# Optimization experiments

Hardware: AMD Instinct MI355X
Metric: run time of the kernel (lower is better)

Reference implementation:

```python
import jax, jax.numpy as jnp
import numpy as np

REWARD_SCALE = 1.0
DIST_NORM = 2
LATENT_DIST_THRESHOLD = 6.0

BS, N_VIEWS, N_PART, F_DIM = 128, 4, 1024, 10


def setup_inputs() -> dict:
    key = jax.random.key(0)
    k1, k2, k3, k4 = jax.random.split(key, 4)
    achieved_goal = jax.random.normal(k1, (BS, N_VIEWS, N_PART, F_DIM), jnp.float32)
    desired_goal = jax.random.normal(k2, (BS, N_VIEWS, N_PART, F_DIM), jnp.float32)
    norm_mean = jax.random.normal(k3, (F_DIM,), jnp.float32)
    norm_std = jax.random.uniform(k4, (F_DIM,), jnp.float32, minval=0.5, maxval=1.5)
    return {"achieved_goal": achieved_goal, "desired_goal": desired_goal,
            "norm_mean": norm_mean, "norm_std": norm_std}


def _pairwise_sqdist(x, y):
    # x: [bs, n, d], y: [bs, m, d] -> [bs, n, m] squared L2 ('l2_simple')
    xx = jnp.sum(x * x, axis=-1)            # [bs, n]
    yy = jnp.sum(y * y, axis=-1)            # [bs, m]
    xy = jnp.einsum('bnd,bmd->bnm', x, y)   # [bs, n, m]
    return xx[:, :, None] + yy[:, None, :] - 2.0 * xy


def _particle_mask(particles):
    # latent_classifier is None -> obj_class_cond = ones -> mask = (1 == 0) = all False
    obj_on = particles[..., -1]
    return jnp.zeros_like(obj_on, dtype=bool)


def reference(achieved_goal, desired_goal, norm_mean, norm_std):
    # unnormalize (particle_normalizer.unnormalize modeled as affine)
    state_particles = achieved_goal * norm_std + norm_mean
    goal_particles = desired_goal * norm_std + norm_mean
    bs, n_views, n_particles, _ = state_particles.shape

    state_mask = _particle_mask(state_particles)   # [bs, nv, np] bool
    goal_mask = _particle_mask(goal_particles)

    # P_mask[b,v,i,j] = state_mask[b,v,i] | goal_mask[b,v,j]
    P_mask = jnp.logical_or(state_mask[..., :, None], goal_mask[..., None, :])

    state_vis = state_particles[..., 5:9]
    state_xy = state_particles[..., :2]
    goal_vis = goal_particles[..., 5:9]
    goal_xy = goal_particles[..., :2]

    inf = jnp.asarray(jnp.inf, state_particles.dtype)
    rewards = []
    for i in range(n_views):
        sxy = state_xy[:, i]                 # [bs, np, 2]
        gxy = goal_xy[:, i]
        gmask_i = goal_mask[:, i]            # [bs, np]
        smask_i = state_mask[:, i]

        P = _pairwise_sqdist(state_vis[:, i], goal_vis[:, i])  # [bs, np_state, np_goal]
        P = jnp.where(P_mask[:, i], inf, P)

        # goal -> state direction: min over state dim (axis 1)
        min_d1 = jnp.min(P, axis=1)                            # [bs, np_goal]
        idx1 = jnp.argmin(P, axis=1)                           # [bs, np_goal]
        d_goal = jnp.take_along_axis(sxy, idx1[..., None], axis=1)  # [bs, np_goal, 2]
        xy_dist_1 = jnp.linalg.norm(gxy - d_goal, ord=DIST_NORM, axis=-1)
        xy_dist_1 = jnp.where(min_d1 > LATENT_DIST_THRESHOLD, 1.0, xy_dist_1)
        xy_dist_1 = jnp.where(gmask_i, 0.0, xy_dist_1)
        n_obj_g = jnp.maximum(jnp.sum(~gmask_i, axis=1), 1)
        reward_g2s = -jnp.sum(xy_dist_1, axis=1) / n_obj_g

        # state -> goal direction: min over goal dim (axis 2)
        min_d2 = jnp.min(P, axis=2)
        idx2 = jnp.argmin(P, axis=2)
        d_state = jnp.take_along_axis(gxy, idx2[..., None], axis=1)
        xy_dist_2 = jnp.linalg.norm(sxy - d_state, ord=DIST_NORM, axis=-1)
        xy_dist_2 = jnp.where(min_d2 > LATENT_DIST_THRESHOLD, 1.0, xy_dist_2)
        xy_dist_2 = jnp.where(smask_i, 0.0, xy_dist_2)
        n_obj_s = jnp.maximum(jnp.sum(~smask_i, axis=1), 1)
        reward_s2g = -jnp.sum(xy_dist_2, axis=1) / n_obj_s

        rv = (reward_g2s + reward_s2g) / 2.0
        no_valid = jnp.logical_or(jnp.all(gmask_i, axis=-1), jnp.all(smask_i, axis=-1))
        rv = jnp.where(no_valid, -1.0, rv)
        rewards.append(rv)

    reward = jnp.mean(jnp.stack(rewards, axis=0), axis=0)   # [bs]
    return REWARD_SCALE * reward[:, None]                    # [bs, 1]
```

## Files before the change

### kernel.cpp

```cpp
#include <hip/hip_runtime.h>
#include <cstdint>
#include <cstddef>

#define NP    1024
#define FD    10
#define NV    4
#define BSZ   128
#define NSET  1024
#define TPB   256
#define RPT   2

#define OFF_CS 16777216

typedef float fv4 __attribute__((ext_vector_type(4)));
typedef const fv4 __attribute__((address_space(4)))* c4p;


extern "C" __global__ __launch_bounds__(256)
void chamfer_stage(const float* __restrict__ ag, const float* __restrict__ dg,
                   const float* __restrict__ nmean, const float* __restrict__ nstd,
                   float* __restrict__ vis2o, float* __restrict__ cso)
{
    __shared__ float raw[NP * FD];
    const int s   = blockIdx.x;
    const int tid = threadIdx.x;
    const float4* src = (const float4*)(((s & 1) ? ag : dg) + (size_t)(s >> 1) * (NP * FD));
    float4* lraw = (float4*)raw;
#pragma unroll
    for (int i = 0; i < 10; ++i)
        lraw[tid + 256 * i] = src[tid + 256 * i];

    float st0 = -2.0f * nstd[5], mn0 = -2.0f * nmean[5];
    float st1 = -2.0f * nstd[6], mn1 = -2.0f * nmean[6];
    float st2 = -2.0f * nstd[7], mn2 = -2.0f * nmean[7];
    float st3 = -2.0f * nstd[8], mn3 = -2.0f * nmean[8];
    __syncthreads();

    fv4*   vout = (fv4*)vis2o + (size_t)s * NP;
    float* cout = cso + (size_t)s * NP;
    for (int n = tid; n < NP; n += 256) {
        float v0 = fmaf(raw[FD * n + 5], st0, mn0);
        float v1 = fmaf(raw[FD * n + 6], st1, mn1);
        float v2 = fmaf(raw[FD * n + 7], st2, mn2);
        float v3 = fmaf(raw[FD * n + 8], st3, mn3);
        fv4 v; v.x = v0; v.y = v1; v.z = v2; v.w = v3;
        vout[n] = v;
        cout[n] = 0.25f * (v0 * v0 + v1 * v1 + v2 * v2 + v3 * v3);
    }
}

extern "C" __global__ __launch_bounds__(TPB, 8)
void chamfer_pairs(const float* __restrict__ vis2, const float* __restrict__ cs,
                   const float* __restrict__ ag, const float* __restrict__ dg,
                   const float* __restrict__ nmean, const float* __restrict__ nstd,
                   float* __restrict__ out )
{
    __shared__ float redbuf[TPB / 64];

    const int bid  = blockIdx.x;
    const int pd   = bid >> 1;
    const int half = bid & 1;
    const int pair = pd >> 1;
    const int d    = pd & 1;
    const int tid  = threadIdx.x;

    c4p cvisS = (c4p)(uintptr_t)(vis2 + (size_t)pd * NP * 4);
    c4p ccsS  = (c4p)(uintptr_t)(cs   + (size_t)pd * NP);
    const float4* cvisV = (const float4*)(vis2 + (size_t)pd * NP * 4);
    const float*  ccsV  = cs + (size_t)pd * NP;
    const float4* rvis4 = (const float4*)(vis2 + (size_t)(pd ^ 1) * NP * 4);
    const float*  rcs   = cs + (size_t)(pd ^ 1) * NP;

    const float* rxyg = ((d == 0) ? ag : dg) + (size_t)pair * (NP * FD);
    const float* cxyg = ((d == 0) ? dg : ag) + (size_t)pair * (NP * FD);

    float4 rv[RPT];
    float  rthr[RPT];
    float  bestd[RPT];
    int    bblk[RPT];
#pragma unroll
    for (int r = 0; r < RPT; ++r) {
        int n = half * 512 + tid + TPB * r;
        float4 t = rvis4[n];
        rv[r] = make_float4(-0.5f * t.x, -0.5f * t.y, -0.5f * t.z, -0.5f * t.w);
        rthr[r] = 6.0f - rcs[n];
        bestd[r] = 3.0e38f;
        bblk[r]  = 0;
    }

    for (int mb8 = 0; mb8 < NP / 8; ++mb8) {
        const int m = mb8 * 8;
        fv4 c0 = cvisS[m + 0];
        fv4 c1 = cvisS[m + 1];
        fv4 c2 = cvisS[m + 2];
        fv4 c3 = cvisS[m + 3];
        fv4 c4 = cvisS[m + 4];
        fv4 c5 = cvisS[m + 5];
        fv4 c6 = cvisS[m + 6];
        fv4 c7 = cvisS[m + 7];
        fv4 csA = ccsS[mb8 * 2 + 0];
        fv4 csB = ccsS[mb8 * 2 + 1];
#pragma unroll
        for (int r = 0; r < RPT; ++r) {
            float4 v = rv[r];
            float d0 = fmaf(v.x, c0.x, csA.x); d0 = fmaf(v.y, c0.y, d0); d0 = fmaf(v.z, c0.z, d0); d0 = fmaf(v.w, c0.w, d0);
            float d1 = fmaf(v.x, c1.x, csA.y); d1 = fmaf(v.y, c1.y, d1); d1 = fmaf(v.z, c1.z, d1); d1 = fmaf(v.w, c1.w, d1);
            float d2 = fmaf(v.x, c2.x, csA.z); d2 = fmaf(v.y, c2.y, d2); d2 = fmaf(v.z, c2.z, d2); d2 = fmaf(v.w, c2.w, d2);
            float d3 = fmaf(v.x, c3.x, csA.w); d3 = fmaf(v.y, c3.y, d3); d3 = fmaf(v.z, c3.z, d3); d3 = fmaf(v.w, c3.w, d3);
            float d4 = fmaf(v.x, c4.x, csB.x); d4 = fmaf(v.y, c4.y, d4); d4 = fmaf(v.z, c4.z, d4); d4 = fmaf(v.w, c4.w, d4);
            float d5 = fmaf(v.x, c5.x, csB.y); d5 = fmaf(v.y, c5.y, d5); d5 = fmaf(v.z, c5.z, d5); d5 = fmaf(v.w, c5.w, d5);
            float d6 = fmaf(v.x, c6.x, csB.z); d6 = fmaf(v.y, c6.y, d6); d6 = fmaf(v.z, c6.z, d6); d6 = fmaf(v.w, c6.w, d6);
            float d7 = fmaf(v.x, c7.x, csB.w); d7 = fmaf(v.y, c7.y, d7); d7 = fmaf(v.z, c7.z, d7); d7 = fmaf(v.w, c7.w, d7);
            float p0 = fminf(fminf(d0, d1), d2);
            float p1 = fminf(fminf(d3, d4), d5);
            float p2 = fminf(d6, d7);
            float bm = fminf(fminf(p0, p1), p2);
            bool lt = bm < bestd[r];
            bestd[r] = fminf(bestd[r], bm);
            bblk[r]  = lt ? m : bblk[r];
        }
    }

    const float std0 = nstd[0], mean0 = nmean[0];
    const float std1 = nstd[1], mean1 = nmean[1];
    float sum = 0.0f;
#pragma unroll
    for (int r = 0; r < RPT; ++r) {
        int n  = half * 512 + tid + TPB * r;
        int mb = bblk[r];
        float4 v = rv[r];
        float cse[8];
#pragma unroll
        for (int j = 0; j < 8; ++j) cse[j] = ccsV[mb + j];
        float dd[8];
#pragma unroll
        for (int j = 0; j < 8; ++j) {
            float4 c = cvisV[mb + j];
            float t = fmaf(v.x, c.x, cse[j]);
            t = fmaf(v.y, c.y, t);
            t = fmaf(v.z, c.z, t);
            t = fmaf(v.w, c.w, t);
            dd[j] = t;
        }
        int sel = 0;
#pragma unroll
        for (int j = 7; j >= 0; --j)
            if (dd[j] == bestd[r]) sel = j;
        int idx = mb + sel;

        float gx = fmaf(cxyg[(size_t)idx * FD + 0], std0, mean0);
        float gy = fmaf(cxyg[(size_t)idx * FD + 1], std1, mean1);
        float ax = fmaf(rxyg[(size_t)n * FD + 0], std0, mean0);
        float ay = fmaf(rxyg[(size_t)n * FD + 1], std1, mean1);
        float dx = ax - gx;
        float dy = ay - gy;
        float dist = sqrtf(dx * dx + dy * dy);
        if (bestd[r] > rthr[r]) dist = 1.0f;
        sum += dist;
    }

    for (int o = 32; o > 0; o >>= 1) sum += __shfl_down(sum, o, 64);
    if ((tid & 63) == 0) redbuf[tid >> 6] = sum;
    __syncthreads();
    if (tid == 0) {
        float s = redbuf[0] + redbuf[1] + redbuf[2] + redbuf[3];
        atomicAdd(&out[pair >> 2], s * (-1.0f / 8192.0f));
    }
}

extern "C" void kernel_launch(void* const* d_in, const int* in_sizes, int n_in,
                              void* d_out, int out_size, void* d_ws, size_t ws_size,
                              hipStream_t stream)
{
    const float* ag = (const float*)d_in[0];
    const float* dg = (const float*)d_in[1];
    const float* nm = (const float*)d_in[2];
    const float* ns = (const float*)d_in[3];

    char*  ws    = (char*)d_ws;
    float* vis2  = (float*)(ws);
    float* csbuf = (float*)(ws + OFF_CS);

    hipMemsetAsync(d_out, 0, BSZ * sizeof(float), stream);
    chamfer_stage<<<NSET, 256, 0, stream>>>(ag, dg, nm, ns, vis2, csbuf);
    chamfer_pairs<<<NSET * 2, TPB, 0, stream>>>(vis2, csbuf, ag, dg, nm, ns, (float*)d_out);
}
```

Baseline: 256.7 us.

## Fuse staging into pair kernel with LDS SoA columns and packed FMA

Drops the separate staging kernel and its workspace round trip. Each block now unnormalizes the column set into LDS in structure-of-arrays form and computes the row vectors directly from the inputs. The inner loop uses 2-wide vector FMA and min, which could map to packed fp32 instructions. The launch shape also changes: 128-thread blocks with 8 rows per thread and 1024 blocks, down from 2048. This cuts the number of blocks and removes the scalar-constant-load path, at the cost of redundant column preprocessing per block and lower occupancy.

```diff
diff --git a/kernel.cpp b/kernel.cpp
--- a/kernel.cpp
+++ b/kernel.cpp
@@ -2,77 +2,48 @@
 #include <cstdint>
 #include <cstddef>
 
-#define NP    1024
-#define FD    10
-#define NV    4
-#define BSZ   128
-#define NSET  1024
-#define TPB   256
-#define RPT   2
+#define NP  1024
+#define FD  10
+#define NV  4
+#define BSZ 128
+#define TPB 128
+#define RPT 8
 
-#define OFF_CS 16777216
+typedef float v2f __attribute__((ext_vector_type(2)));
+typedef float v4f __attribute__((ext_vector_type(4)));
 
-typedef float fv4 __attribute__((ext_vector_type(4)));
-typedef const fv4 __attribute__((address_space(4)))* c4p;
-
-
-extern "C" __global__ __launch_bounds__(256)
-void chamfer_stage(const float* __restrict__ ag, const float* __restrict__ dg,
-                   const float* __restrict__ nmean, const float* __restrict__ nstd,
-                   float* __restrict__ vis2o, float* __restrict__ cso)
-{
-    __shared__ float raw[NP * FD];
-    const int s   = blockIdx.x;
-    const int tid = threadIdx.x;
-    const float4* src = (const float4*)(((s & 1) ? ag : dg) + (size_t)(s >> 1) * (NP * FD));
-    float4* lraw = (float4*)raw;
-#pragma unroll
-    for (int i = 0; i < 10; ++i)
-        lraw[tid + 256 * i] = src[tid + 256 * i];
-
-    float st0 = -2.0f * nstd[5], mn0 = -2.0f * nmean[5];
-    float st1 = -2.0f * nstd[6], mn1 = -2.0f * nmean[6];
-    float st2 = -2.0f * nstd[7], mn2 = -2.0f * nmean[7];
-    float st3 = -2.0f * nstd[8], mn3 = -2.0f * nmean[8];
-    __syncthreads();
-
-    fv4*   vout = (fv4*)vis2o + (size_t)s * NP;
-    float* cout = cso + (size_t)s * NP;
-    for (int n = tid; n < NP; n += 256) {
-        float v0 = fmaf(raw[FD * n + 5], st0, mn0);
-        float v1 = fmaf(raw[FD * n + 6], st1, mn1);
-        float v2 = fmaf(raw[FD * n + 7], st2, mn2);
-        float v3 = fmaf(raw[FD * n + 8], st3, mn3);
-        fv4 v; v.x = v0; v.y = v1; v.z = v2; v.w = v3;
-        vout[n] = v;
-        cout[n] = 0.25f * (v0 * v0 + v1 * v1 + v2 * v2 + v3 * v3);
-    }
-}
-
-extern "C" __global__ __launch_bounds__(TPB, 8)
-void chamfer_pairs(const float* __restrict__ vis2, const float* __restrict__ cs,
-                   const float* __restrict__ ag, const float* __restrict__ dg,
+extern "C" __global__ __launch_bounds__(TPB, 2)
+void chamfer_pairs(const float* __restrict__ ag, const float* __restrict__ dg,
                    const float* __restrict__ nmean, const float* __restrict__ nstd,
                    float* __restrict__ out )
 {
-    __shared__ float redbuf[TPB / 64];
+    __shared__ float cxF[NP], cyF[NP], czF[NP], cwF[NP], csF[NP];
+    __shared__ float red[TPB / 64];
 
     const int bid  = blockIdx.x;
-    const int pd   = bid >> 1;
-    const int half = bid & 1;
-    const int pair = pd >> 1;
-    const int d    = pd & 1;
+    const int pair = bid >> 1;
+    const int d    = bid & 1;
     const int tid  = threadIdx.x;
 
-    c4p cvisS = (c4p)(uintptr_t)(vis2 + (size_t)pd * NP * 4);
-    c4p ccsS  = (c4p)(uintptr_t)(cs   + (size_t)pd * NP);
-    const float4* cvisV = (const float4*)(vis2 + (size_t)pd * NP * 4);
-    const float*  ccsV  = cs + (size_t)pd * NP;
-    const float4* rvis4 = (const float4*)(vis2 + (size_t)(pd ^ 1) * NP * 4);
-    const float*  rcs   = cs + (size_t)(pd ^ 1) * NP;
+    const float* rowsrc = ((d == 0) ? ag : dg) + (size_t)pair * (NP * FD);
+    const float* colsrc = ((d == 0) ? dg : ag) + (size_t)pair * (NP * FD);
 
-    const float* rxyg = ((d == 0) ? ag : dg) + (size_t)pair * (NP * FD);
-    const float* cxyg = ((d == 0) ? dg : ag) + (size_t)pair * (NP * FD);
+    const float s5 = -2.0f * nstd[5], m5 = -2.0f * nmean[5];
+    const float s6 = -2.0f * nstd[6], m6 = -2.0f * nmean[6];
+    const float s7 = -2.0f * nstd[7], m7 = -2.0f * nmean[7];
+    const float s8 = -2.0f * nstd[8], m8 = -2.0f * nmean[8];
+    const float std0 = nstd[0], mean0 = nmean[0];
+    const float std1 = nstd[1], mean1 = nmean[1];
+
+    for (int m = tid; m < NP; m += TPB) {
+        const float* p = colsrc + (size_t)m * FD;
+        float t0 = fmaf(p[5], s5, m5);
+        float t1 = fmaf(p[6], s6, m6);
+        float t2 = fmaf(p[7], s7, m7);
+        float t3 = fmaf(p[8], s8, m8);
+        cxF[m] = t0; cyF[m] = t1; czF[m] = t2; cwF[m] = t3;
+        csF[m] = 0.25f * (t0 * t0 + t1 * t1 + t2 * t2 + t3 * t3);
+    }
 
     float4 rv[RPT];
     float  rthr[RPT];
@@ -80,66 +51,79 @@
     int    bblk[RPT];
 #pragma unroll
     for (int r = 0; r < RPT; ++r) {
-        int n = half * 512 + tid + TPB * r;
-        float4 t = rvis4[n];
-        rv[r] = make_float4(-0.5f * t.x, -0.5f * t.y, -0.5f * t.z, -0.5f * t.w);
-        rthr[r] = 6.0f - rcs[n];
+        int n = tid + TPB * r;
+        const float* p = rowsrc + (size_t)n * FD;
+        float t0 = fmaf(p[5], s5, m5);
+        float t1 = fmaf(p[6], s6, m6);
+        float t2 = fmaf(p[7], s7, m7);
+        float t3 = fmaf(p[8], s8, m8);
+        rv[r] = make_float4(-0.5f * t0, -0.5f * t1, -0.5f * t2, -0.5f * t3);
+        float rss = 0.25f * (t0 * t0 + t1 * t1 + t2 * t2 + t3 * t3);
+        rthr[r] = 6.0f - rss;
         bestd[r] = 3.0e38f;
         bblk[r]  = 0;
     }
+    __syncthreads();
 
-    for (int mb8 = 0; mb8 < NP / 8; ++mb8) {
-        const int m = mb8 * 8;
-        fv4 c0 = cvisS[m + 0];
-        fv4 c1 = cvisS[m + 1];
-        fv4 c2 = cvisS[m + 2];
-        fv4 c3 = cvisS[m + 3];
-        fv4 c4 = cvisS[m + 4];
-        fv4 c5 = cvisS[m + 5];
-        fv4 c6 = cvisS[m + 6];
-        fv4 c7 = cvisS[m + 7];
-        fv4 csA = ccsS[mb8 * 2 + 0];
-        fv4 csB = ccsS[mb8 * 2 + 1];
+    const v4f* X4 = (const v4f*)cxF;
+    const v4f* Y4 = (const v4f*)cyF;
+    const v4f* Z4 = (const v4f*)czF;
+    const v4f* W4 = (const v4f*)cwF;
+    const v4f* S4 = (const v4f*)csF;
+
+#pragma unroll 2
+    for (int g = 0; g < NP / 8; ++g) {
+        const int m = g * 8;
+        v4f xA = X4[2 * g], xB = X4[2 * g + 1];
+        v4f yA = Y4[2 * g], yB = Y4[2 * g + 1];
+        v4f zA = Z4[2 * g], zB = Z4[2 * g + 1];
+        v4f wA = W4[2 * g], wB = W4[2 * g + 1];
+        v4f cA = S4[2 * g], cB = S4[2 * g + 1];
 #pragma unroll
         for (int r = 0; r < RPT; ++r) {
-            float4 v = rv[r];
-            float d0 = fmaf(v.x, c0.x, csA.x); d0 = fmaf(v.y, c0.y, d0); d0 = fmaf(v.z, c0.z, d0); d0 = fmaf(v.w, c0.w, d0);
-            float d1 = fmaf(v.x, c1.x, csA.y); d1 = fmaf(v.y, c1.y, d1); d1 = fmaf(v.z, c1.z, d1); d1 = fmaf(v.w, c1.w, d1);
-            float d2 = fmaf(v.x, c2.x, csA.z); d2 = fmaf(v.y, c2.y, d2); d2 = fmaf(v.z, c2.z, d2); d2 = fmaf(v.w, c2.w, d2);
-            float d3 = fmaf(v.x, c3.x, csA.w); d3 = fmaf(v.y, c3.y, d3); d3 = fmaf(v.z, c3.z, d3); d3 = fmaf(v.w, c3.w, d3);
-            float d4 = fmaf(v.x, c4.x, csB.x); d4 = fmaf(v.y, c4.y, d4); d4 = fmaf(v.z, c4.z, d4); d4 = fmaf(v.w, c4.w, d4);
-            float d5 = fmaf(v.x, c5.x, csB.y); d5 = fmaf(v.y, c5.y, d5); d5 = fmaf(v.z, c5.z, d5); d5 = fmaf(v.w, c5.w, d5);
-            float d6 = fmaf(v.x, c6.x, csB.z); d6 = fmaf(v.y, c6.y, d6); d6 = fmaf(v.z, c6.z, d6); d6 = fmaf(v.w, c6.w, d6);
-            float d7 = fmaf(v.x, c7.x, csB.w); d7 = fmaf(v.y, c7.y, d7); d7 = fmaf(v.z, c7.z, d7); d7 = fmaf(v.w, c7.w, d7);
-            float p0 = fminf(fminf(d0, d1), d2);
-            float p1 = fminf(fminf(d3, d4), d5);
-            float p2 = fminf(d6, d7);
-            float bm = fminf(fminf(p0, p1), p2);
+            v2f vx = {rv[r].x, rv[r].x};
+            v2f vy = {rv[r].y, rv[r].y};
+            v2f vz = {rv[r].z, rv[r].z};
+            v2f vw = {rv[r].w, rv[r].w};
+            v2f q0 = __builtin_elementwise_fma(vx, xA.lo, cA.lo);
+            q0 = __builtin_elementwise_fma(vy, yA.lo, q0);
+            q0 = __builtin_elementwise_fma(vz, zA.lo, q0);
+            q0 = __builtin_elementwise_fma(vw, wA.lo, q0);
+            v2f q1 = __builtin_elementwise_fma(vx, xA.hi, cA.hi);
+            q1 = __builtin_elementwise_fma(vy, yA.hi, q1);
+            q1 = __builtin_elementwise_fma(vz, zA.hi, q1);
+            q1 = __builtin_elementwise_fma(vw, wA.hi, q1);
+            v2f q2 = __builtin_elementwise_fma(vx, xB.lo, cB.lo);
+            q2 = __builtin_elementwise_fma(vy, yB.lo, q2);
+            q2 = __builtin_elementwise_fma(vz, zB.lo, q2);
+            q2 = __builtin_elementwise_fma(vw, wB.lo, q2);
+            v2f q3 = __builtin_elementwise_fma(vx, xB.hi, cB.hi);
+            q3 = __builtin_elementwise_fma(vy, yB.hi, q3);
+            q3 = __builtin_elementwise_fma(vz, zB.hi, q3);
+            q3 = __builtin_elementwise_fma(vw, wB.hi, q3);
+            v2f m01 = __builtin_elementwise_min(q0, q1);
+            v2f m23 = __builtin_elementwise_min(q2, q3);
+            v2f mm  = __builtin_elementwise_min(m01, m23);
+            float bm = fminf(mm.x, mm.y);
             bool lt = bm < bestd[r];
             bestd[r] = fminf(bestd[r], bm);
             bblk[r]  = lt ? m : bblk[r];
         }
     }
 
-    const float std0 = nstd[0], mean0 = nmean[0];
-    const float std1 = nstd[1], mean1 = nmean[1];
     float sum = 0.0f;
 #pragma unroll
     for (int r = 0; r < RPT; ++r) {
-        int n  = half * 512 + tid + TPB * r;
+        int n  = tid + TPB * r;
         int mb = bblk[r];
         float4 v = rv[r];
-        float cse[8];
-#pragma unroll
-        for (int j = 0; j < 8; ++j) cse[j] = ccsV[mb + j];
         float dd[8];
 #pragma unroll
         for (int j = 0; j < 8; ++j) {
-            float4 c = cvisV[mb + j];
-            float t = fmaf(v.x, c.x, cse[j]);
-            t = fmaf(v.y, c.y, t);
-            t = fmaf(v.z, c.z, t);
-            t = fmaf(v.w, c.w, t);
+            float t = fmaf(v.x, cxF[mb + j], csF[mb + j]);
+            t = fmaf(v.y, cyF[mb + j], t);
+            t = fmaf(v.z, czF[mb + j], t);
+            t = fmaf(v.w, cwF[mb + j], t);
             dd[j] = t;
         }
         int sel = 0;
@@ -148,10 +132,10 @@
             if (dd[j] == bestd[r]) sel = j;
         int idx = mb + sel;
 
-        float gx = fmaf(cxyg[(size_t)idx * FD + 0], std0, mean0);
-        float gy = fmaf(cxyg[(size_t)idx * FD + 1], std1, mean1);
-        float ax = fmaf(rxyg[(size_t)n * FD + 0], std0, mean0);
-        float ay = fmaf(rxyg[(size_t)n * FD + 1], std1, mean1);
+        float gx = fmaf(colsrc[(size_t)idx * FD + 0], std0, mean0);
+        float gy = fmaf(colsrc[(size_t)idx * FD + 1], std1, mean1);
+        float ax = fmaf(rowsrc[(size_t)n * FD + 0], std0, mean0);
+        float ay = fmaf(rowsrc[(size_t)n * FD + 1], std1, mean1);
         float dx = ax - gx;
         float dy = ay - gy;
         float dist = sqrtf(dx * dx + dy * dy);
@@ -160,10 +144,10 @@
     }
 
     for (int o = 32; o > 0; o >>= 1) sum += __shfl_down(sum, o, 64);
-    if ((tid & 63) == 0) redbuf[tid >> 6] = sum;
+    if ((tid & 63) == 0) red[tid >> 6] = sum;
     __syncthreads();
     if (tid == 0) {
-        float s = redbuf[0] + redbuf[1] + redbuf[2] + redbuf[3];
+        float s = red[0] + red[1];
         atomicAdd(&out[pair >> 2], s * (-1.0f / 8192.0f));
     }
 }
@@ -177,11 +161,6 @@
     const float* nm = (const float*)d_in[2];
     const float* ns = (const float*)d_in[3];
 
-    char*  ws    = (char*)d_ws;
-    float* vis2  = (float*)(ws);
-    float* csbuf = (float*)(ws + OFF_CS);
-
     hipMemsetAsync(d_out, 0, BSZ * sizeof(float), stream);
-    chamfer_stage<<<NSET, 256, 0, stream>>>(ag, dg, nm, ns, vis2, csbuf);
-    chamfer_pairs<<<NSET * 2, TPB, 0, stream>>>(vis2, csbuf, ag, dg, nm, ns, (float*)d_out);
+    chamfer_pairs<<<BSZ * NV * 2, TPB, 0, stream>>>(ag, dg, nm, ns, (float*)d_out);
 }
```

Result: faster. 228.2 us (-11.1%).
